# Kernel tuning notes

Hardware: AMD Instinct MI355X
Metric: run time of the kernel (lower is better)

The kernel has to match this reference:

```python
import jax, jax.numpy as jnp
import numpy as np


def setup_inputs() -> dict:
    key = jax.random.key(0)
    x = jax.random.normal(key, (128, 256, 32, 32), dtype=jnp.float32)
    return {"x": x, "topk": 5}


def reference(x, topk):
    B = x.shape[0]
    flat = x.reshape(B, -1)                      # [B, N]
    _, idx = jax.lax.top_k(flat, topk)           # [B, k] indices into N
    out = jnp.zeros_like(flat)
    out = out.at[jnp.arange(B)[:, None], idx].set(1.0)
    return out.reshape(x.shape)
```

## Files before the change

### kernel.cpp

```cpp
#include <hip/hip_runtime.h>
#include <limits.h>
#include <math.h>
#include <stdint.h>

#define BROWS 128
#define NCOLS (256 * 32 * 32)
#define K 5
#define BPR 16
#define TPB 256
#define CHUNK (NCOLS / BPR)
#define F4T (CHUNK / 4 / TPB)
#define NW (TPB / 64)

typedef float v4f __attribute__((ext_vector_type(4)));

__device__ __forceinline__ uint64_t make_key(float f, uint32_t idx) {
    uint32_t u = __float_as_uint(f);
    u = (u & 0x80000000u) ? ~u : (u | 0x80000000u);
    return ((uint64_t)u << 32) | (uint32_t)(~idx);
}
__device__ __forceinline__ uint32_t key_idx(uint64_t k) { return ~(uint32_t)k; }
__device__ __forceinline__ float key_val(uint64_t k) {
    uint32_t u = (uint32_t)(k >> 32);
    u = (u & 0x80000000u) ? (u & 0x7FFFFFFFu) : ~u;
    return __uint_as_float(u);
}

#define KEY_NEG_INF 0x007FFFFF00000000ULL

__device__ __forceinline__ void insert5(uint64_t (&key)[K], uint64_t c) {
    if (c > key[K - 1]) {
        key[K - 1] = c;
#pragma unroll
        for (int s = K - 1; s > 0; --s) {
            if (key[s] > key[s - 1]) {
                uint64_t t = key[s]; key[s] = key[s - 1]; key[s - 1] = t;
            }
        }
    }
}

__device__ __forceinline__ void wave_reduce5(uint64_t (&key)[K]) {
#pragma unroll
    for (int off = 1; off < 64; off <<= 1) {
        uint64_t ok[K];
#pragma unroll
        for (int k = 0; k < K; ++k)
            ok[k] = __shfl_xor((unsigned long long)key[k], off, 64);
#pragma unroll
        for (int k = 0; k < K; ++k) insert5(key, ok[k]);
    }
}

__global__ __launch_bounds__(TPB) void wta_pass(const float* __restrict__ x,
                                                float* __restrict__ out,
                                                uint64_t* __restrict__ cand) {
    const int gb  = blockIdx.x;
    const int row = gb / BPR;
    const int blk = gb % BPR;
    const size_t base = (size_t)gb * CHUNK;
    const float4* __restrict__ x4 = (const float4*)(x + base);
    v4f* __restrict__ o4 = (v4f*)(out + base);
    const int t = threadIdx.x;
    const v4f z = {0.f, 0.f, 0.f, 0.f};

    uint64_t key[K];
#pragma unroll
    for (int k = 0; k < K; ++k) key[k] = KEY_NEG_INF;
    float vth = -INFINITY;
    const uint32_t ebase = (uint32_t)blk * CHUNK;

#pragma unroll
    for (int h = 0; h < 2; ++h) {
        float4 r[F4T / 2];
#pragma unroll
        for (int j = 0; j < F4T / 2; ++j)
            r[j] = x4[t + (h * (F4T / 2) + j) * TPB];
#pragma unroll
        for (int j = 0; j < F4T / 2; ++j)
            __builtin_nontemporal_store(z, &o4[t + (h * (F4T / 2) + j) * TPB]);
#pragma unroll
        for (int j = 0; j < F4T / 2; ++j) {
            const float4 d = r[j];
            const float m = fmaxf(fmaxf(d.x, d.y), fmaxf(d.z, d.w));
            if (m >= vth) {
                const uint32_t e = ebase + (uint32_t)(t + (h * (F4T / 2) + j) * TPB) * 4u;
                const float vs[4] = {d.x, d.y, d.z, d.w};
#pragma unroll
                for (int c = 0; c < 4; ++c) insert5(key, make_key(vs[c], e + c));
                vth = key_val(key[K - 1]);
            }
        }
    }

    wave_reduce5(key);

    __shared__ uint64_t sk[NW * K];
    const int lane = t & 63, w = t >> 6;
    if (lane == 0) {
#pragma unroll
        for (int k = 0; k < K; ++k) sk[w * K + k] = key[k];
    }
    __syncthreads();
    if (t < 64) {
        uint64_t fk[K];
#pragma unroll
        for (int k = 0; k < K; ++k) fk[k] = KEY_NEG_INF;
        if (t < NW * K) fk[0] = sk[t];
        wave_reduce5(fk);
        if (t == 0) {
#pragma unroll
            for (int k = 0; k < K; ++k)
                cand[((size_t)row * BPR + blk) * K + k] = fk[k];
        }
    }
}

__global__ __launch_bounds__(64) void wta_final(const uint64_t* __restrict__ cand,
                                                float* __restrict__ out) {
    const int row = blockIdx.x, lane = threadIdx.x;
    const uint64_t* __restrict__ c = cand + (size_t)row * BPR * K;

    uint64_t key[K];
#pragma unroll
    for (int k = 0; k < K; ++k) key[k] = KEY_NEG_INF;
#pragma unroll
    for (int i = 0; i < 2; ++i) {
        const int j = i * 64 + lane;
        if (j < BPR * K) insert5(key, c[j]);
    }

    wave_reduce5(key);

    if (lane == 0) {
#pragma unroll
        for (int k = 0; k < K; ++k)
            if (key[k] != KEY_NEG_INF)
                out[(size_t)row * NCOLS + key_idx(key[k])] = 1.0f;
    }
}

extern "C" void kernel_launch(void* const* d_in, const int* in_sizes, int n_in,
                              void* d_out, int out_size, void* d_ws, size_t ws_size,
                              hipStream_t stream) {
    const float* x = (const float*)d_in[0];
    float* out = (float*)d_out;

    uint64_t* cand = (uint64_t*)d_ws;

    wta_pass<<<BROWS * BPR, TPB, 0, stream>>>(x, out, cand);
    wta_final<<<BROWS, 64, 0, stream>>>(cand, out);
}
```

Before: 264.9 us.

## Prefilter candidates with wave-wide top-5 threshold and double blocks per row

Each thread now computes its per-float4 maxima and the thread max. A float-only wave shuffle reduction of those maxima gives a fifth-largest threshold, and only elements at or above that threshold are inserted into the per-thread 64-bit key top-5. This replaces the running per-thread threshold, which diverged and did much insertion work early on. Blocks per row go from 16 to 32, halving per-block work and doubling the grid. The cost is an extra shuffle reduction per wave, more registers to hold all loaded data at once, and more candidates for the final kernel to merge.

```diff
diff --git a/kernel.cpp b/kernel.cpp
--- a/kernel.cpp
+++ b/kernel.cpp
@@ -6,7 +6,7 @@
 #define BROWS 128
 #define NCOLS (256 * 32 * 32)
 #define K 5
-#define BPR 16
+#define BPR 32
 #define TPB 256
 #define CHUNK (NCOLS / BPR)
 #define F4T (CHUNK / 4 / TPB)
@@ -20,11 +20,6 @@
     return ((uint64_t)u << 32) | (uint32_t)(~idx);
 }
 __device__ __forceinline__ uint32_t key_idx(uint64_t k) { return ~(uint32_t)k; }
-__device__ __forceinline__ float key_val(uint64_t k) {
-    uint32_t u = (uint32_t)(k >> 32);
-    u = (u & 0x80000000u) ? (u & 0x7FFFFFFFu) : ~u;
-    return __uint_as_float(u);
-}
 
 #define KEY_NEG_INF 0x007FFFFF00000000ULL
 
@@ -52,6 +47,16 @@
     }
 }
 
+__device__ __forceinline__ void insert5f(float (&v)[K], float c) {
+    if (c > v[K - 1]) {
+        v[K - 1] = c;
+#pragma unroll
+        for (int s = K - 1; s > 0; --s) {
+            if (v[s] > v[s - 1]) { float t = v[s]; v[s] = v[s - 1]; v[s - 1] = t; }
+        }
+    }
+}
+
 __global__ __launch_bounds__(TPB) void wta_pass(const float* __restrict__ x,
                                                 float* __restrict__ out,
                                                 uint64_t* __restrict__ cand) {
@@ -64,32 +69,47 @@
     const int t = threadIdx.x;
     const v4f z = {0.f, 0.f, 0.f, 0.f};
 
+    float4 d[F4T];
+#pragma unroll
+    for (int j = 0; j < F4T; ++j) d[j] = x4[t + j * TPB];
+#pragma unroll
+    for (int j = 0; j < F4T; ++j)
+        __builtin_nontemporal_store(z, &o4[t + j * TPB]);
+
+    float mj[F4T];
+#pragma unroll
+    for (int j = 0; j < F4T; ++j)
+        mj[j] = fmaxf(fmaxf(d[j].x, d[j].y), fmaxf(d[j].z, d[j].w));
+    float M = -INFINITY;
+#pragma unroll
+    for (int j = 0; j < F4T; ++j) M = fmaxf(M, mj[j]);
+
+    float v[K];
+    v[0] = M;
+#pragma unroll
+    for (int k = 1; k < K; ++k) v[k] = -INFINITY;
+#pragma unroll
+    for (int off = 1; off < 64; off <<= 1) {
+        float ov[K];
+#pragma unroll
+        for (int k = 0; k < K; ++k) ov[k] = __shfl_xor(v[k], off, 64);
+#pragma unroll
+        for (int k = 0; k < K; ++k) insert5f(v, ov[k]);
+    }
+    const float T = v[K - 1];
+
     uint64_t key[K];
 #pragma unroll
     for (int k = 0; k < K; ++k) key[k] = KEY_NEG_INF;
-    float vth = -INFINITY;
     const uint32_t ebase = (uint32_t)blk * CHUNK;
-
 #pragma unroll
-    for (int h = 0; h < 2; ++h) {
-        float4 r[F4T / 2];
+    for (int j = 0; j < F4T; ++j) {
+        if (mj[j] >= T) {
+            const uint32_t e = ebase + (uint32_t)(t + j * TPB) * 4u;
+            const float vs[4] = {d[j].x, d[j].y, d[j].z, d[j].w};
 #pragma unroll
-        for (int j = 0; j < F4T / 2; ++j)
-            r[j] = x4[t + (h * (F4T / 2) + j) * TPB];
-#pragma unroll
-        for (int j = 0; j < F4T / 2; ++j)
-            __builtin_nontemporal_store(z, &o4[t + (h * (F4T / 2) + j) * TPB]);
-#pragma unroll
-        for (int j = 0; j < F4T / 2; ++j) {
-            const float4 d = r[j];
-            const float m = fmaxf(fmaxf(d.x, d.y), fmaxf(d.z, d.w));
-            if (m >= vth) {
-                const uint32_t e = ebase + (uint32_t)(t + (h * (F4T / 2) + j) * TPB) * 4u;
-                const float vs[4] = {d.x, d.y, d.z, d.w};
-#pragma unroll
-                for (int c = 0; c < 4; ++c) insert5(key, make_key(vs[c], e + c));
-                vth = key_val(key[K - 1]);
-            }
+            for (int c = 0; c < 4; ++c)
+                if (vs[c] >= T) insert5(key, make_key(vs[c], e + c));
         }
     }
 
@@ -125,7 +145,7 @@
 #pragma unroll
     for (int k = 0; k < K; ++k) key[k] = KEY_NEG_INF;
 #pragma unroll
-    for (int i = 0; i < 2; ++i) {
+    for (int i = 0; i < (BPR * K + 63) / 64; ++i) {
         const int j = i * 64 + lane;
         if (j < BPR * K) insert5(key, c[j]);
     }
```

New measurement: 250.7 us. 1.06x faster.
